# Kernel optimization log

Measured on AMD Instinct MI355X. Metric: run time of the kernel, lower is better.

The kernel has to match this reference:

```python
import math
import jax, jax.numpy as jnp
import numpy as np

B, S, D, H = 2, 2048, 1024, 16
DK = D // H  # 64


def _rope_tables(seq_len, d_k):
    inv_freq = 1.0 / (10000.0 ** (jnp.arange(0, d_k, 2, dtype=jnp.float32) / d_k))
    t = jnp.arange(seq_len, dtype=jnp.float32)
    freqs = t[:, None] * inv_freq[None, :]          # [S, d_k/2]
    emb = jnp.concatenate([freqs, freqs], axis=-1)  # [S, d_k]
    return jnp.cos(emb), jnp.sin(emb)


def _rotate_half(x):
    x1, x2 = jnp.split(x, 2, axis=-1)
    return jnp.concatenate([-x2, x1], axis=-1)


def setup_inputs() -> dict:
    key = jax.random.key(0)
    ks = jax.random.split(key, 11)
    sc = 1.0 / math.sqrt(D)
    inp = {
        'query': jax.random.normal(ks[0], (B, S, D), jnp.float32),
        'key': jax.random.normal(ks[1], (B, S, D), jnp.float32),
        'value': jax.random.normal(ks[2], (B, S, D), jnp.float32),
        'mask': jnp.tril(jnp.ones((S, S), bool))[None, None, :, :],  # causal [1,1,S,S]
        'Wq': jax.random.normal(ks[3], (D, D), jnp.float32) * sc,
        'bq': jnp.zeros((D,), jnp.float32),
        'Wk': jax.random.normal(ks[4], (D, D), jnp.float32) * sc,
        'bk': jnp.zeros((D,), jnp.float32),
        'Wv': jax.random.normal(ks[5], (D, D), jnp.float32) * sc,
        'bv': jnp.zeros((D,), jnp.float32),
        'Wo': jax.random.normal(ks[6], (D, D), jnp.float32) * sc,
        'bo': jnp.zeros((D,), jnp.float32),
    }
    return inp


def reference(query, key, value, mask, Wq, bq, Wk, bk, Wv, bv, Wo, bo):
    b, s, d = query.shape
    # QKV projections -> [b, H, s, DK]
    def proj(x, W, bias):
        y = x @ W.T + bias
        return y.reshape(b, s, H, DK).transpose(0, 2, 1, 3)
    q = proj(query, Wq, bq)
    k = proj(key, Wk, bk)
    v = proj(value, Wv, bv)
    # inline RoPE
    cos, sin = _rope_tables(s, DK)          # [s, DK]
    cos = cos[None, None]; sin = sin[None, None]
    q = q * cos + _rotate_half(q) * sin
    k = k * cos + _rotate_half(k) * sin
    # naive O(N^2) attention (dropout disabled: eval-mode reference)
    scores = jnp.einsum('bhqd,bhkd->bhqk', q, k) / math.sqrt(DK)
    scores = jnp.where(mask, scores, jnp.float32(-1e9))
    p = jax.nn.softmax(scores, axis=-1)
    x = jnp.einsum('bhqk,bhkd->bhqd', p, v)
    x = x.transpose(0, 2, 1, 3).reshape(b, s, d)
    return x @ Wo.T + bo
```

## Files before the change

### kernel.cpp

```cpp
#include <hip/hip_runtime.h>
#include <hip/hip_bf16.h>
#include <math.h>

typedef unsigned short u16;
typedef unsigned int u32;
typedef __attribute__((ext_vector_type(4))) float f32x4;
typedef __attribute__((ext_vector_type(4))) short bf16x4;
typedef __attribute__((ext_vector_type(8))) short bf16x8;
typedef __attribute__((ext_vector_type(8))) unsigned short u16x8;

constexpr int Bc = 2, Sc = 2048, Dc = 1024, Hc = 16, DKc = 64, Mc = 4096;

__device__ __forceinline__ u16 f2bf(float f) {
  __hip_bfloat16 h = __float2bfloat16(f);
  return __builtin_bit_cast(u16, h);
}

__device__ __forceinline__ void gll16(const u16* g, const u16* l) {
  __builtin_amdgcn_global_load_lds((const __attribute__((address_space(1))) void*)g,
                                   (__attribute__((address_space(3))) void*)l, 16, 0, 0);
}

__device__ __forceinline__ bf16x8 frag_swz(const u16* tile, int row, int col) {
  const int sw = (row & 7) << 3;
  const int base = row * 64 + col;
  bf16x4 lo = *(const bf16x4*)(tile + (base ^ sw));
  bf16x4 hi = *(const bf16x4*)(tile + ((base + 16) ^ sw));
  return __builtin_shufflevector(lo, hi, 0, 1, 2, 3, 4, 5, 6, 7);
}

__global__ __launch_bounds__(256) void cast_many(
    const float* __restrict__ i0, const float* __restrict__ i1,
    const float* __restrict__ i2, const float* __restrict__ i3,
    u16* __restrict__ o0, u16* __restrict__ o1,
    u16* __restrict__ o2, u16* __restrict__ o3, int n8)
{
  const int z = blockIdx.y;
  const float* in = z == 0 ? i0 : z == 1 ? i1 : z == 2 ? i2 : i3;
  u16* out = z == 0 ? o0 : z == 1 ? o1 : z == 2 ? o2 : o3;
  const int i = blockIdx.x * 256 + threadIdx.x;
  if (i >= n8) return;
  const float4* p = (const float4*)in + (size_t)i * 2;
  const float4 a = p[0], b = p[1];
  u16x8 o;
  o[0] = f2bf(a.x); o[1] = f2bf(a.y); o[2] = f2bf(a.z); o[3] = f2bf(a.w);
  o[4] = f2bf(b.x); o[5] = f2bf(b.y); o[6] = f2bf(b.z); o[7] = f2bf(b.w);
  ((u16x8*)out)[i] = o;
}

__device__ __forceinline__ void gemm_core(
    const u16* __restrict__ X, const u16* __restrict__ W,
    u16* smem, int row0, int col0, f32x4 (&acc)[2][4])
{
  const int tid = threadIdx.x;
  const int w = tid >> 6, lane = tid & 63;
  const int l15 = lane & 15, l4 = lane >> 4;
  const int wr = w >> 1, wc = w & 1;

  auto stage = [&](int buf, int k0) {
    u16* dA = smem + buf * 4096;
    u16* dB = smem + 8192 + buf * 8192;
#pragma unroll
    for (int s = 0; s < 2; ++s) {
      const int c = s * 256 + w * 64 + lane;
      const int r = c >> 3, cc = (c & 7) ^ (r & 7);
      gll16(X + (size_t)(row0 + r) * Dc + k0 + cc * 8, dA + (s * 256 + w * 64) * 8);
    }
#pragma unroll
    for (int s = 0; s < 4; ++s) {
      const int c = s * 256 + w * 64 + lane;
      const int r = c >> 3, cc = (c & 7) ^ (r & 7);
      gll16(W + (size_t)(col0 + r) * Dc + k0 + cc * 8, dB + (s * 256 + w * 64) * 8);
    }
  };

  stage(0, 0);
  __syncthreads();

  for (int kt = 0; kt < Dc / 64; ++kt) {
    const int cur = kt & 1;
    if (kt + 1 < Dc / 64) stage(cur ^ 1, (kt + 1) * 64);
    const u16* At = smem + cur * 4096;
    const u16* Bt = smem + 8192 + cur * 8192;
#pragma unroll
    for (int ks = 0; ks < 2; ++ks) {
      bf16x8 af[2], bfr[4];
#pragma unroll
      for (int m = 0; m < 2; ++m)
        af[m] = frag_swz(At, wr * 32 + m * 16 + l15, ks * 32 + l4 * 4);
#pragma unroll
      for (int n = 0; n < 4; ++n)
        bfr[n] = frag_swz(Bt, wc * 64 + n * 16 + l15, ks * 32 + l4 * 4);
#pragma unroll
      for (int m = 0; m < 2; ++m)
#pragma unroll
        for (int n = 0; n < 4; ++n)
          acc[m][n] = __builtin_amdgcn_mfma_f32_16x16x32_bf16(af[m], bfr[n], acc[m][n], 0, 0, 0);
    }
    __syncthreads();
  }
}

__global__ __launch_bounds__(256) void gemm_qkv(
    const u16* __restrict__ xq, const u16* __restrict__ xk, const u16* __restrict__ xv,
    const u16* __restrict__ wq, const u16* __restrict__ wk, const u16* __restrict__ wv,
    const float* __restrict__ bq, const float* __restrict__ bk, const float* __restrict__ bv,
    u16* __restrict__ Qb, u16* __restrict__ Kb, u16* __restrict__ Vt)
{
  __shared__ u16 smem[24576];
  const int z = blockIdx.z;
  const u16* X = z == 0 ? xq : z == 1 ? xk : xv;
  const u16* W = z == 0 ? wq : z == 1 ? wk : wv;
  const float* bias = z == 0 ? bq : z == 1 ? bk : bv;

  const int tid = threadIdx.x;
  const int w = tid >> 6, lane = tid & 63;
  const int l15 = lane & 15, l4 = lane >> 4;
  const int wr = w >> 1, wc = w & 1;
  const int row0 = blockIdx.x * 64;
  const int col0 = blockIdx.y * 128;

  f32x4 acc[2][4] = {};
  gemm_core(X, W, smem, row0, col0, acc);

  if (z < 2) {
    u16* Out = z == 0 ? Qb : Kb;
    const int h = (col0 >> 6) + wc;
#pragma unroll
    for (int m = 0; m < 2; ++m)
#pragma unroll
      for (int i = 0; i < 4; ++i) {
        const int row = row0 + wr * 32 + m * 16 + 4 * l4 + i;
        const int srow = row & (Sc - 1);
        const size_t obase = ((size_t)((row >> 11) * Hc + h) * Sc + srow) * DKc;
        float vv[4];
#pragma unroll
        for (int n = 0; n < 4; ++n)
          vv[n] = acc[m][n][i] + bias[col0 + wc * 64 + n * 16 + l15];
        float cs[2], sn[2];
#pragma unroll
        for (int hf = 0; hf < 2; ++hf) {
          const int jj = hf * 16 + l15;
          const float ang = (float)srow * exp2f((float)jj * (-13.287712379549449f / 32.0f));
          sincosf(ang, &sn[hf], &cs[hf]);
        }
#pragma unroll
        for (int n = 0; n < 4; ++n) {
          const float rot = (n < 2) ? -vv[n ^ 2] : vv[n ^ 2];
          const float o = vv[n] * cs[n & 1] + rot * sn[n & 1];
          Out[obase + n * 16 + l15] = f2bf(o);
        }
      }
  } else {
    u16* T = smem;
    __syncthreads();
#pragma unroll
    for (int m = 0; m < 2; ++m)
#pragma unroll
      for (int i = 0; i < 4; ++i) {
        const int r = wr * 32 + m * 16 + 4 * l4 + i;
#pragma unroll
        for (int n = 0; n < 4; ++n) {
          const int c = wc * 64 + n * 16 + l15;
          T[c * 72 + r] = f2bf(acc[m][n][i] + bias[col0 + c]);
        }
      }
    __syncthreads();
    const int bidx = row0 >> 11, srow0 = row0 & (Sc - 1);
    const int c = tid >> 1, rq = (tid & 1) * 32;
    const int h = (col0 >> 6) + (c >> 6);
    const int dk = c & 63;
    u16* gdst = Vt + ((size_t)(bidx * Hc + h) * DKc + dk) * Sc + srow0 + rq;
#pragma unroll
    for (int u = 0; u < 4; ++u)
      *(u16x8*)(gdst + u * 8) = *(const u16x8*)&T[c * 72 + rq + u * 8];
  }
}

__global__ __launch_bounds__(256) void gemm_out(
    const u16* __restrict__ X, const u16* __restrict__ W,
    const float* __restrict__ bias, float* __restrict__ Out)
{
  __shared__ u16 smem[24576];
  const int tid = threadIdx.x;
  const int w = tid >> 6, lane = tid & 63;
  const int l15 = lane & 15, l4 = lane >> 4;
  const int wr = w >> 1, wc = w & 1;
  const int row0 = blockIdx.x * 64;
  const int col0 = blockIdx.y * 128;

  f32x4 acc[2][4] = {};
  gemm_core(X, W, smem, row0, col0, acc);

#pragma unroll
  for (int m = 0; m < 2; ++m)
#pragma unroll
    for (int i = 0; i < 4; ++i) {
      const int row = row0 + wr * 32 + m * 16 + 4 * l4 + i;
#pragma unroll
      for (int n = 0; n < 4; ++n) {
        const int col = col0 + wc * 64 + n * 16 + l15;
        Out[(size_t)row * Dc + col] = acc[m][n][i] + bias[col];
      }
    }
}

__global__ __launch_bounds__(256) void attn_mfma(
    const u16* __restrict__ Qb, const u16* __restrict__ Kb,
    const u16* __restrict__ Vt, u16* __restrict__ Xb)
{
  __shared__ u16 smem[20480];
  u16* Qs = smem;

  const int tid = threadIdx.x;
  const int w = tid >> 6, lane = tid & 63;
  const int l15 = lane & 15, l4 = lane >> 4;
  const int qt = gridDim.x - 1 - blockIdx.x;
  const int bh = blockIdx.y;
  const int q0 = qt * 64;
  const u16* Qg = Qb + ((size_t)bh * Sc + q0) * DKc;
  const u16* Kg = Kb + (size_t)bh * Sc * DKc;
  const u16* Vg = Vt + (size_t)bh * DKc * Sc;

#pragma unroll
  for (int s = 0; s < 2; ++s) {
    const int c = s * 256 + w * 64 + lane;
    const int r = c >> 3, cc = (c & 7) ^ (r & 7);
    gll16(Qg + (size_t)r * DKc + cc * 8, Qs + (s * 256 + w * 64) * 8);
  }
  auto stageKV = [&](int buf, int k0) {
    u16* Kd = smem + 4096 + buf * 4096;
    u16* Vd = smem + 12288 + buf * 4096;
#pragma unroll
    for (int s = 0; s < 2; ++s) {
      const int c = s * 256 + w * 64 + lane;
      const int r = c >> 3, cc = (c & 7) ^ (r & 7);
      gll16(Kg + (size_t)(k0 + r) * DKc + cc * 8, Kd + (s * 256 + w * 64) * 8);
      gll16(Vg + (size_t)r * Sc + k0 + cc * 8,   Vd + (s * 256 + w * 64) * 8);
    }
  };
  stageKV(0, 0);
  __syncthreads();

  bf16x8 aq[2];
#pragma unroll
  for (int ks = 0; ks < 2; ++ks)
    aq[ks] = frag_swz(Qs, w * 16 + l15, ks * 32 + l4 * 4);

  f32x4 aco[4] = {};
  float mreg = -INFINITY, lreg = 0.f;
  constexpr float C2 = 0.18033688011112042f;

  const int nk = qt + 1;
  for (int kt = 0; kt < nk; ++kt) {
    const int cur = kt & 1;
    if (kt + 1 < nk) stageKV(cur ^ 1, (kt + 1) * 64);
    const u16* Kt = smem + 4096 + cur * 4096;
    const u16* Vc = smem + 12288 + cur * 4096;

    f32x4 acs[4] = {};
#pragma unroll
    for (int ks = 0; ks < 2; ++ks) {
      bf16x8 bk[4];
#pragma unroll
      for (int n = 0; n < 4; ++n)
        bk[n] = frag_swz(Kt, n * 16 + l15, ks * 32 + l4 * 4);
#pragma unroll
      for (int n = 0; n < 4; ++n)
        acs[n] = __builtin_amdgcn_mfma_f32_16x16x32_bf16(bk[n], aq[ks], acs[n], 0, 0, 0);
    }

    const bool mtile = (kt == qt);
    const int k0 = kt * 64;
    const int q = q0 + w * 16 + l15;
    float rm = -INFINITY;
#pragma unroll
    for (int n = 0; n < 4; ++n)
#pragma unroll
      for (int i = 0; i < 4; ++i) {
        float s = acs[n][i] * C2;
        if (mtile && (k0 + n * 16 + 4 * l4 + i) > q) s = -1e30f;
        acs[n][i] = s;
        rm = fmaxf(rm, s);
      }
    rm = fmaxf(rm, __shfl_xor(rm, 16, 64));
    rm = fmaxf(rm, __shfl_xor(rm, 32, 64));

    const bool need = __any(rm > mreg + 8.0f);
    float corr = 1.f;
    if (need) {
      const float mnew = fmaxf(mreg, rm);
      corr = exp2f(mreg - mnew);
      mreg = mnew;
    }
    float rs = 0.f;
#pragma unroll
    for (int n = 0; n < 4; ++n)
#pragma unroll
      for (int i = 0; i < 4; ++i) {
        const float p = exp2f(acs[n][i] - mreg);
        acs[n][i] = p;
        rs += p;
      }
    rs += __shfl_xor(rs, 16, 64);
    rs += __shfl_xor(rs, 32, 64);
    lreg = lreg * corr + rs;
    if (need) {
#pragma unroll
      for (int i = 0; i < 4; ++i) {
        const float c = __shfl(corr, 4 * l4 + i, 64);
#pragma unroll
        for (int n = 0; n < 4; ++n) aco[n][i] *= c;
      }
    }

    bf16x8 pa[2];
#pragma unroll
    for (int ks = 0; ks < 2; ++ks) {
      bf16x8 t;
#pragma unroll
      for (int j = 0; j < 8; ++j)
        t[j] = (short)f2bf(acs[ks * 2 + (j >> 2)][j & 3]);
      pa[ks] = t;
    }

#pragma unroll
    for (int ks = 0; ks < 2; ++ks) {
      bf16x8 bv[4];
#pragma unroll
      for (int n = 0; n < 4; ++n)
        bv[n] = frag_swz(Vc, n * 16 + l15, ks * 32 + l4 * 4);
#pragma unroll
      for (int n = 0; n < 4; ++n)
        aco[n] = __builtin_amdgcn_mfma_f32_16x16x32_bf16(pa[ks], bv[n], aco[n], 0, 0, 0);
    }
    __syncthreads();
  }

  const int bidx = bh >> 4, h = bh & 15;
  const float invl = 1.0f / lreg;
#pragma unroll
  for (int i = 0; i < 4; ++i) {
    const int q = q0 + w * 16 + 4 * l4 + i;
    const float inv = __shfl(invl, 4 * l4 + i, 64);
#pragma unroll
    for (int n = 0; n < 4; ++n)
      Xb[((size_t)bidx * Sc + q) * Dc + h * DKc + n * 16 + l15] = f2bf(aco[n][i] * inv);
  }
}

extern "C" void kernel_launch(void* const* d_in, const int* in_sizes, int n_in,
                              void* d_out, int out_size, void* d_ws, size_t ws_size,
                              hipStream_t stream) {
  const float* query = (const float*)d_in[0];
  const float* key   = (const float*)d_in[1];
  const float* value = (const float*)d_in[2];
  const float* Wq = (const float*)d_in[4];
  const float* bq = (const float*)d_in[5];
  const float* Wk = (const float*)d_in[6];
  const float* bk = (const float*)d_in[7];
  const float* Wv = (const float*)d_in[8];
  const float* bv = (const float*)d_in[9];
  const float* Wo = (const float*)d_in[10];
  const float* bo = (const float*)d_in[11];

  const size_t MD = (size_t)Mc * Dc;
  const size_t DD = (size_t)Dc * Dc;
  u16* xq = (u16*)d_ws;
  u16* xk = xq + MD;
  u16* xv = xk + MD;
  u16* wq = xv + MD;
  u16* wk = wq + DD;
  u16* wv = wk + DD;
  u16* wo = wv + DD;
  u16* Qb = wo + DD;
  u16* Kb = Qb + MD;
  u16* Vt = Kb + MD;
  u16* Xb = Vt + MD;

  cast_many<<<dim3(MD / 2048, 3), 256, 0, stream>>>(
      query, key, value, nullptr, xq, xk, xv, nullptr, (int)(MD / 8));
  cast_many<<<dim3(DD / 2048, 4), 256, 0, stream>>>(
      Wq, Wk, Wv, Wo, wq, wk, wv, wo, (int)(DD / 8));

  gemm_qkv<<<dim3(Mc / 64, Dc / 128, 3), 256, 0, stream>>>(
      xq, xk, xv, wq, wk, wv, bq, bk, bv, Qb, Kb, Vt);
  attn_mfma<<<dim3(Sc / 64, Bc * Hc), 256, 0, stream>>>(Qb, Kb, Vt, Xb);
  gemm_out<<<dim3(Mc / 64, Dc / 128), 256, 0, stream>>>(Xb, wo, bo, (float*)d_out);
}
```

Measured before the change: 272.2 us.

## Enlarge GEMM tiles to 128x128 with remapped grid and triple-buffer attention K/V

The GEMMs move to 512-thread blocks with 128x128 output tiles, and block indices are remapped so neighbouring blocks share input panels, which should raise data reuse and L2 locality. The attention kernel adds a swizzled block-to-(head, q-tile) mapping and a three-slot K/V ring. The QK^T for the next tile is issued before the softmax of the current one, so loads and MFMA overlap. The risks are higher register pressure and more LDS per block, which lowers occupancy, and the new multi-buffer index arithmetic is complex.

```diff
diff --git a/kernel.cpp b/kernel.cpp
--- a/kernel.cpp
+++ b/kernel.cpp
@@ -48,6 +48,13 @@
   ((u16x8*)out)[i] = o;
 }
 
+__device__ __forceinline__ void gemm_remap(int& row0, int& col0) {
+  const int flat = blockIdx.x + gridDim.x * blockIdx.y;
+  const int loc = flat >> 3;
+  row0 = ((flat & 7) * 4 + (loc & 3)) * 128;
+  col0 = (loc >> 2) * 128;
+}
+
 __device__ __forceinline__ void gemm_core(
     const u16* __restrict__ X, const u16* __restrict__ W,
     u16* smem, int row0, int col0, f32x4 (&acc)[2][4])
@@ -58,19 +65,15 @@
   const int wr = w >> 1, wc = w & 1;
 
   auto stage = [&](int buf, int k0) {
-    u16* dA = smem + buf * 4096;
-    u16* dB = smem + 8192 + buf * 8192;
+    u16* dA = smem + buf * 8192;
+    u16* dB = smem + 16384 + buf * 8192;
 #pragma unroll
     for (int s = 0; s < 2; ++s) {
-      const int c = s * 256 + w * 64 + lane;
-      const int r = c >> 3, cc = (c & 7) ^ (r & 7);
-      gll16(X + (size_t)(row0 + r) * Dc + k0 + cc * 8, dA + (s * 256 + w * 64) * 8);
-    }
-#pragma unroll
-    for (int s = 0; s < 4; ++s) {
-      const int c = s * 256 + w * 64 + lane;
-      const int r = c >> 3, cc = (c & 7) ^ (r & 7);
-      gll16(W + (size_t)(col0 + r) * Dc + k0 + cc * 8, dB + (s * 256 + w * 64) * 8);
+      const int c = s * 512 + w * 64 + lane;
+      const int r = c >> 3;
+      const int cc = (c & 7) ^ (r & 7);
+      gll16(X + (size_t)(row0 + r) * Dc + k0 + cc * 8, dA + (s * 512 + w * 64) * 8);
+      gll16(W + (size_t)(col0 + r) * Dc + k0 + cc * 8, dB + (s * 512 + w * 64) * 8);
     }
   };
 
@@ -80,8 +83,8 @@
   for (int kt = 0; kt < Dc / 64; ++kt) {
     const int cur = kt & 1;
     if (kt + 1 < Dc / 64) stage(cur ^ 1, (kt + 1) * 64);
-    const u16* At = smem + cur * 4096;
-    const u16* Bt = smem + 8192 + cur * 8192;
+    const u16* At = smem + cur * 8192;
+    const u16* Bt = smem + 16384 + cur * 8192;
 #pragma unroll
     for (int ks = 0; ks < 2; ++ks) {
       bf16x8 af[2], bfr[4];
@@ -101,13 +104,13 @@
   }
 }
 
-__global__ __launch_bounds__(256) void gemm_qkv(
+__global__ __launch_bounds__(512) void gemm_qkv(
     const u16* __restrict__ xq, const u16* __restrict__ xk, const u16* __restrict__ xv,
     const u16* __restrict__ wq, const u16* __restrict__ wk, const u16* __restrict__ wv,
     const float* __restrict__ bq, const float* __restrict__ bk, const float* __restrict__ bv,
     u16* __restrict__ Qb, u16* __restrict__ Kb, u16* __restrict__ Vt)
 {
-  __shared__ u16 smem[24576];
+  __shared__ u16 smem[4 * 128 * 64];
   const int z = blockIdx.z;
   const u16* X = z == 0 ? xq : z == 1 ? xk : xv;
   const u16* W = z == 0 ? wq : z == 1 ? wk : wv;
@@ -117,8 +120,8 @@
   const int w = tid >> 6, lane = tid & 63;
   const int l15 = lane & 15, l4 = lane >> 4;
   const int wr = w >> 1, wc = w & 1;
-  const int row0 = blockIdx.x * 64;
-  const int col0 = blockIdx.y * 128;
+  int row0, col0;
+  gemm_remap(row0, col0);
 
   f32x4 acc[2][4] = {};
   gemm_core(X, W, smem, row0, col0, acc);
@@ -162,32 +165,32 @@
 #pragma unroll
         for (int n = 0; n < 4; ++n) {
           const int c = wc * 64 + n * 16 + l15;
-          T[c * 72 + r] = f2bf(acc[m][n][i] + bias[col0 + c]);
+          T[c * 132 + r] = f2bf(acc[m][n][i] + bias[col0 + c]);
         }
       }
     __syncthreads();
     const int bidx = row0 >> 11, srow0 = row0 & (Sc - 1);
-    const int c = tid >> 1, rq = (tid & 1) * 32;
+    const int c = tid >> 2, rq = (tid & 3) * 32;
     const int h = (col0 >> 6) + (c >> 6);
     const int dk = c & 63;
     u16* gdst = Vt + ((size_t)(bidx * Hc + h) * DKc + dk) * Sc + srow0 + rq;
 #pragma unroll
     for (int u = 0; u < 4; ++u)
-      *(u16x8*)(gdst + u * 8) = *(const u16x8*)&T[c * 72 + rq + u * 8];
+      *(u16x8*)(gdst + u * 8) = *(const u16x8*)&T[c * 132 + rq + u * 8];
   }
 }
 
-__global__ __launch_bounds__(256) void gemm_out(
+__global__ __launch_bounds__(512) void gemm_out(
     const u16* __restrict__ X, const u16* __restrict__ W,
     const float* __restrict__ bias, float* __restrict__ Out)
 {
-  __shared__ u16 smem[24576];
+  __shared__ u16 smem[4 * 128 * 64];
   const int tid = threadIdx.x;
   const int w = tid >> 6, lane = tid & 63;
   const int l15 = lane & 15, l4 = lane >> 4;
   const int wr = w >> 1, wc = w & 1;
-  const int row0 = blockIdx.x * 64;
-  const int col0 = blockIdx.y * 128;
+  int row0, col0;
+  gemm_remap(row0, col0);
 
   f32x4 acc[2][4] = {};
   gemm_core(X, W, smem, row0, col0, acc);
@@ -209,34 +212,38 @@
     const u16* __restrict__ Qb, const u16* __restrict__ Kb,
     const u16* __restrict__ Vt, u16* __restrict__ Xb)
 {
-  __shared__ u16 smem[20480];
-  u16* Qs = smem;
+  __shared__ u16 smem[24576];
+  u16* Qs = smem + 16384;
 
   const int tid = threadIdx.x;
   const int w = tid >> 6, lane = tid & 63;
   const int l15 = lane & 15, l4 = lane >> 4;
-  const int qt = gridDim.x - 1 - blockIdx.x;
-  const int bh = blockIdx.y;
+
+  const int d = blockIdx.x + gridDim.x * blockIdx.y;
+  const int loc = d >> 3;
+  const int bh = (d & 7) * 4 + (loc & 3);
+  const int qt = 31 - (loc >> 2);
   const int q0 = qt * 64;
   const u16* Qg = Qb + ((size_t)bh * Sc + q0) * DKc;
   const u16* Kg = Kb + (size_t)bh * Sc * DKc;
   const u16* Vg = Vt + (size_t)bh * DKc * Sc;
+  const int nk = qt + 1;
 
 #pragma unroll
   for (int s = 0; s < 2; ++s) {
-    const int c = s * 256 + w * 64 + lane;
+    const int c = s * 256 + tid;
     const int r = c >> 3, cc = (c & 7) ^ (r & 7);
-    gll16(Qg + (size_t)r * DKc + cc * 8, Qs + (s * 256 + w * 64) * 8);
+    gll16(Qg + (size_t)r * DKc + cc * 8, Qs + c * 8);
   }
   auto stageKV = [&](int buf, int k0) {
-    u16* Kd = smem + 4096 + buf * 4096;
-    u16* Vd = smem + 12288 + buf * 4096;
+    u16* Kd = smem + (buf == 0 ? 0 : buf == 1 ? 8192 : 16384);
+    u16* Vd = smem + (buf == 0 ? 4096 : buf == 1 ? 12288 : 20480);
 #pragma unroll
     for (int s = 0; s < 2; ++s) {
-      const int c = s * 256 + w * 64 + lane;
+      const int c = s * 256 + tid;
       const int r = c >> 3, cc = (c & 7) ^ (r & 7);
-      gll16(Kg + (size_t)(k0 + r) * DKc + cc * 8, Kd + (s * 256 + w * 64) * 8);
-      gll16(Vg + (size_t)r * Sc + k0 + cc * 8,   Vd + (s * 256 + w * 64) * 8);
+      gll16(Kg + (size_t)(k0 + r) * DKc + cc * 8, Kd + c * 8);
+      gll16(Vg + (size_t)r * Sc + k0 + cc * 8,   Vd + c * 8);
     }
   };
   stageKV(0, 0);
@@ -247,40 +254,50 @@
   for (int ks = 0; ks < 2; ++ks)
     aq[ks] = frag_swz(Qs, w * 16 + l15, ks * 32 + l4 * 4);
 
+  if (nk > 1) stageKV(1, 64);
+
+  auto QK = [&](f32x4 (&dst)[4], int buf) {
+    const u16* Kt = smem + (buf == 0 ? 0 : buf == 1 ? 8192 : 16384);
+#pragma unroll
+    for (int ks = 0; ks < 2; ++ks) {
+      bf16x8 bk[4];
+#pragma unroll
+      for (int n = 0; n < 4; ++n)
+        bk[n] = frag_swz(Kt, n * 16 + l15, ks * 32 + l4 * 4);
+#pragma unroll
+      for (int n = 0; n < 4; ++n)
+        dst[n] = __builtin_amdgcn_mfma_f32_16x16x32_bf16(bk[n], aq[ks], dst[n], 0, 0, 0);
+    }
+  };
+
+  f32x4 sA[4] = {}, sB[4] = {};
+  QK(sA, 0);
+
   f32x4 aco[4] = {};
   float mreg = -INFINITY, lreg = 0.f;
   constexpr float C2 = 0.18033688011112042f;
 
-  const int nk = qt + 1;
-  for (int kt = 0; kt < nk; ++kt) {
-    const int cur = kt & 1;
-    if (kt + 1 < nk) stageKV(cur ^ 1, (kt + 1) * 64);
-    const u16* Kt = smem + 4096 + cur * 4096;
-    const u16* Vc = smem + 12288 + cur * 4096;
-
-    f32x4 acs[4] = {};
-#pragma unroll
-    for (int ks = 0; ks < 2; ++ks) {
-      bf16x8 bk[4];
-#pragma unroll
-      for (int n = 0; n < 4; ++n)
-        bk[n] = frag_swz(Kt, n * 16 + l15, ks * 32 + l4 * 4);
-#pragma unroll
-      for (int n = 0; n < 4; ++n)
-        acs[n] = __builtin_amdgcn_mfma_f32_16x16x32_bf16(bk[n], aq[ks], acs[n], 0, 0, 0);
-    }
-
-    const bool mtile = (kt == qt);
-    const int k0 = kt * 64;
+  auto ITER = [&](int t, f32x4 (&cur)[4], f32x4 (&nxt)[4]) {
+    __syncthreads();
+    const int tb = t - (t / 3) * 3;
+    if (t + 2 < nk) stageKV(tb + 2 >= 3 ? tb - 1 : tb + 2, (t + 2) * 64);
+    if (t + 1 < nk) {
+#pragma unroll
+      for (int n = 0; n < 4; ++n) nxt[n] = f32x4{0.f, 0.f, 0.f, 0.f};
+      QK(nxt, tb + 1 >= 3 ? tb - 2 : tb + 1);
+    }
+
+    const bool mtile = (t == nk - 1);
+    const int k0t = t * 64;
     const int q = q0 + w * 16 + l15;
     float rm = -INFINITY;
 #pragma unroll
     for (int n = 0; n < 4; ++n)
 #pragma unroll
       for (int i = 0; i < 4; ++i) {
-        float s = acs[n][i] * C2;
-        if (mtile && (k0 + n * 16 + 4 * l4 + i) > q) s = -1e30f;
-        acs[n][i] = s;
+        float s = cur[n][i] * C2;
+        if (mtile && (k0t + n * 16 + 4 * l4 + i) > q) s = -1e30f;
+        cur[n][i] = s;
         rm = fmaxf(rm, s);
       }
     rm = fmaxf(rm, __shfl_xor(rm, 16, 64));
@@ -298,8 +315,8 @@
     for (int n = 0; n < 4; ++n)
 #pragma unroll
       for (int i = 0; i < 4; ++i) {
-        const float p = exp2f(acs[n][i] - mreg);
-        acs[n][i] = p;
+        const float p = exp2f(cur[n][i] - mreg);
+        cur[n][i] = p;
         rs += p;
       }
     rs += __shfl_xor(rs, 16, 64);
@@ -317,13 +334,14 @@
     bf16x8 pa[2];
 #pragma unroll
     for (int ks = 0; ks < 2; ++ks) {
-      bf16x8 t;
+      bf16x8 tt;
 #pragma unroll
       for (int j = 0; j < 8; ++j)
-        t[j] = (short)f2bf(acs[ks * 2 + (j >> 2)][j & 3]);
-      pa[ks] = t;
-    }
-
+        tt[j] = (short)f2bf(cur[ks * 2 + (j >> 2)][j & 3]);
+      pa[ks] = tt;
+    }
+
+    const u16* Vc = smem + (tb == 0 ? 4096 : tb == 1 ? 12288 : 20480);
 #pragma unroll
     for (int ks = 0; ks < 2; ++ks) {
       bf16x8 bv[4];
@@ -334,7 +352,14 @@
       for (int n = 0; n < 4; ++n)
         aco[n] = __builtin_amdgcn_mfma_f32_16x16x32_bf16(pa[ks], bv[n], aco[n], 0, 0, 0);
     }
-    __syncthreads();
+  };
+
+  int t = 0;
+  while (true) {
+    ITER(t, sA, sB);
+    if (++t >= nk) break;
+    ITER(t, sB, sA);
+    if (++t >= nk) break;
   }
 
   const int bidx = bh >> 4, h = bh & 15;
@@ -383,8 +408,8 @@
   cast_many<<<dim3(DD / 2048, 4), 256, 0, stream>>>(
       Wq, Wk, Wv, Wo, wq, wk, wv, wo, (int)(DD / 8));
 
-  gemm_qkv<<<dim3(Mc / 64, Dc / 128, 3), 256, 0, stream>>>(
+  gemm_qkv<<<dim3(32, 8, 3), 512, 0, stream>>>(
       xq, xk, xv, wq, wk, wv, bq, bk, bv, Qb, Kb, Vt);
-  attn_mfma<<<dim3(Sc / 64, Bc * Hc), 256, 0, stream>>>(Qb, Kb, Vt, Xb);
-  gemm_out<<<dim3(Mc / 64, Dc / 128), 256, 0, stream>>>(Xb, wo, bo, (float*)d_out);
-}
+  attn_mfma<<<dim3(32, 32), 256, 0, stream>>>(Qb, Kb, Vt, Xb);
+  gemm_out<<<dim3(32, 8), 512, 0, stream>>>(Xb, wo, bo, (float*)d_out);
+}
```

Result: faster. 232.3 us (-14.7%).
